# Kernel optimization log

Measured on AMD Instinct MI355X. Metric: run time of the kernel, lower is better.

Reference implementation:

```python
import jax, jax.numpy as jnp
import numpy as np

N = 100000
E = 640000
C = 128
ALPHA = 0.1
BETA = 0.5
RESIDUAL = False


def setup_inputs() -> dict:
    key = jax.random.key(0)
    k1, k2, k3, k4, k5 = jax.random.split(key, 5)
    stdv = 1.0 / np.sqrt(C)
    x = jax.random.normal(k1, (N, C), dtype=jnp.float32)
    init_x = jax.random.normal(k2, (N, C), dtype=jnp.float32)
    weight = jax.random.uniform(k3, (C, C), dtype=jnp.float32, minval=-stdv, maxval=stdv)
    edge_index = jax.random.randint(k4, (2, E), 0, N, dtype=jnp.int64)
    edge_attr = jax.random.uniform(k5, (E,), dtype=jnp.float32)
    return {"x": x, "edge_index": edge_index, "edge_attr": edge_attr,
            "init_x": init_x, "weight": weight}


def reference(x, edge_index, edge_attr, init_x, weight):
    row, col = edge_index[0], edge_index[1]
    # spmm: out[row] += edge_attr * x[col]  (gather-scale-scatter)
    msgs = edge_attr[:, None] * x[col]                 # [E, C]
    hidden = jax.ops.segment_sum(msgs, row, num_segments=x.shape[0])  # [N, C]
    hidden = (1.0 - ALPHA) * hidden + ALPHA * init_x
    h = BETA * jnp.matmul(hidden, weight) + (1.0 - BETA) * hidden
    if RESIDUAL:
        h = h + x
    return h
```

## Files before the change

kernel.cpp:

```cpp
#include <hip/hip_runtime.h>


#define ALPHA 0.1f
#define BETA  0.5f
#define C_DIM 128
#define PAD   32
#define WSCALE (32767.0f / 0.9f)
#define WDEC   (0.9f / 32767.0f)

typedef __attribute__((ext_vector_type(8))) short short8v;
typedef __attribute__((ext_vector_type(4))) float f32x4;

__device__ inline unsigned bf16rn(float f) {
    unsigned u = __float_as_uint(f);
    return (u + 0x7FFFu + ((u >> 16) & 1u)) >> 16;
}
__device__ inline unsigned pack2(float lo, float hi) {
    return bf16rn(lo) | (bf16rn(hi) << 16);
}

__global__ void k_prep(const float4* __restrict__ x4, uint4* __restrict__ xb, int n8x,
                       const float* __restrict__ W, ushort* __restrict__ Wt,
                       const int* __restrict__ ei, const float* __restrict__ attr,
                       int* __restrict__ cnt, unsigned* __restrict__ recs, int E,
                       int nbin) {
    int b = blockIdx.x;
    if (b < nbin) {
        int base = b * 1024 + threadIdx.x;
#pragma unroll
        for (int k = 0; k < 4; ++k) {
            int e = base + k * 256;
            if (e < E) {
                int row = ei[e];
                int col = ei[E + e];
                float w = (1.0f - ALPHA) * attr[e];
                int wb = (int)(w * WSCALE + 0.5f);
                if (wb > 32767) wb = 32767;
                if (wb < 0) wb = 0;
                int pos = atomicAdd(&cnt[row], 1);
                if (pos >= PAD) pos = PAD - 1;
                __builtin_nontemporal_store(((unsigned)col << 15) | (unsigned)wb,
                                            &recs[(size_t)row * PAD + pos]);
            }
        }
    } else {
        int i = (b - nbin) * 256 + threadIdx.x;
        if (i < n8x) {
            float4 a = x4[2 * i], c = x4[2 * i + 1];
            uint4 o;
            o.x = pack2(a.x, a.y); o.y = pack2(a.z, a.w);
            o.z = pack2(c.x, c.y); o.w = pack2(c.z, c.w);
            xb[i] = o;
        } else if (i < n8x + C_DIM * C_DIM) {
            int j = i - n8x;
            int n = j >> 7, k = j & 127;
            float v = BETA * W[k * C_DIM + n] + ((k == n) ? (1.0f - BETA) : 0.0f);
            Wt[j] = (ushort)bf16rn(v);
        }
    }
}

__device__ inline void fma8(float* acc, float a, uint4 v) {
    acc[0] += a * __uint_as_float(v.x << 16);
    acc[1] += a * __uint_as_float(v.x & 0xffff0000u);
    acc[2] += a * __uint_as_float(v.y << 16);
    acc[3] += a * __uint_as_float(v.y & 0xffff0000u);
    acc[4] += a * __uint_as_float(v.z << 16);
    acc[5] += a * __uint_as_float(v.z & 0xffff0000u);
    acc[6] += a * __uint_as_float(v.w << 16);
    acc[7] += a * __uint_as_float(v.w & 0xffff0000u);
}

template <int MODE>
__global__ __launch_bounds__(256)
void k_gather(const void* __restrict__ xsrc, const int* __restrict__ cnt,
              const unsigned* __restrict__ recs, uint4* __restrict__ hb, int N) {
    const int tid = threadIdx.x;
    long r = (long)blockIdx.x * 16 + (tid >> 4);
    if (r >= N) return;
    const int l = tid & 15;

    float acc[8] = {0.f, 0.f, 0.f, 0.f, 0.f, 0.f, 0.f, 0.f};
    int end = cnt[r];
    if (end > PAD) end = PAD;
    const uint4* rp = (const uint4*)(recs + (size_t)r * PAD);

    for (int k = 0; k < end; k += 8) {
        uint4 qa = rp[(k >> 2) + 0];
        uint4 qb = rp[(k >> 2) + 1];
        int   c0 = (int)(qa.x >> 15), c1 = (int)(qa.y >> 15);
        int   c2 = (int)(qa.z >> 15), c3 = (int)(qa.w >> 15);
        int   c4 = (int)(qb.x >> 15), c5 = (int)(qb.y >> 15);
        int   c6 = (int)(qb.z >> 15), c7 = (int)(qb.w >> 15);
        float w0 = (float)(qa.x & 0x7fffu) * WDEC;
        float w1 = (float)(qa.y & 0x7fffu) * WDEC;
        float w2 = (float)(qa.z & 0x7fffu) * WDEC;
        float w3 = (float)(qa.w & 0x7fffu) * WDEC;
        float w4 = (float)(qb.x & 0x7fffu) * WDEC;
        float w5 = (float)(qb.y & 0x7fffu) * WDEC;
        float w6 = (float)(qb.z & 0x7fffu) * WDEC;
        float w7 = (float)(qb.w & 0x7fffu) * WDEC;
        if (k + 1 >= end) { c1 = 0; w1 = 0.f; }
        if (k + 2 >= end) { c2 = 0; w2 = 0.f; }
        if (k + 3 >= end) { c3 = 0; w3 = 0.f; }
        if (k + 4 >= end) { c4 = 0; w4 = 0.f; }
        if (k + 5 >= end) { c5 = 0; w5 = 0.f; }
        if (k + 6 >= end) { c6 = 0; w6 = 0.f; }
        if (k + 7 >= end) { c7 = 0; w7 = 0.f; }
        if (MODE == 1) {
            const uint4* xb4 = (const uint4*)xsrc;
            uint4 v0 = xb4[(size_t)c0 * 16 + l];
            uint4 v1 = xb4[(size_t)c1 * 16 + l];
            uint4 v2 = xb4[(size_t)c2 * 16 + l];
            uint4 v3 = xb4[(size_t)c3 * 16 + l];
            uint4 v4 = xb4[(size_t)c4 * 16 + l];
            uint4 v5 = xb4[(size_t)c5 * 16 + l];
            uint4 v6 = xb4[(size_t)c6 * 16 + l];
            uint4 v7 = xb4[(size_t)c7 * 16 + l];
            fma8(acc, w0, v0); fma8(acc, w1, v1);
            fma8(acc, w2, v2); fma8(acc, w3, v3);
            fma8(acc, w4, v4); fma8(acc, w5, v5);
            fma8(acc, w6, v6); fma8(acc, w7, v7);
        } else {
            const float4* x4 = (const float4*)xsrc;
            int cc[8] = {c0, c1, c2, c3, c4, c5, c6, c7};
            float ww[8] = {w0, w1, w2, w3, w4, w5, w6, w7};
#pragma unroll
            for (int j = 0; j < 8; ++j) {
                const float4* xr = x4 + (size_t)cc[j] * 32 + 2 * l;
                float4 a0 = xr[0], a1 = xr[1];
                float w = ww[j];
                acc[0] += w * a0.x; acc[1] += w * a0.y;
                acc[2] += w * a0.z; acc[3] += w * a0.w;
                acc[4] += w * a1.x; acc[5] += w * a1.y;
                acc[6] += w * a1.z; acc[7] += w * a1.w;
            }
        }
    }
    uint4 o;
    o.x = pack2(acc[0], acc[1]);
    o.y = pack2(acc[2], acc[3]);
    o.z = pack2(acc[4], acc[5]);
    o.w = pack2(acc[6], acc[7]);
    hb[(size_t)r * 16 + l] = o;
}

__global__ __launch_bounds__(256)
void k_gemm(const uint4* __restrict__ hb, const float4* __restrict__ if4,
            const ushort* __restrict__ Wt, float* __restrict__ out, int N) {
    const uint4* W16 = (const uint4*)Wt;
    int lane = threadIdx.x & 63;
    int wv   = threadIdx.x >> 6;
    int m = lane & 15, g = lane >> 4;
    long R0 = (long)blockIdx.x * 128 + wv * 32;

    f32x4 acc[2][8];
#pragma unroll
    for (int t = 0; t < 2; ++t)
#pragma unroll
        for (int nt = 0; nt < 8; ++nt) acc[t][nt] = (f32x4){0.f, 0.f, 0.f, 0.f};

#pragma unroll
    for (int ks = 0; ks < 4; ++ks) {
        short8v a[2];
#pragma unroll
        for (int t = 0; t < 2; ++t) {
            long r = R0 + t * 16 + m;
            if (r >= N) r = N - 1;
            uint4 hv = hb[r * 16 + ks * 4 + g];
            float4 i0 = if4[r * 32 + ks * 8 + g * 2];
            float4 i1 = if4[r * 32 + ks * 8 + g * 2 + 1];
            float f0 = __uint_as_float(hv.x << 16)         + ALPHA * i0.x;
            float f1 = __uint_as_float(hv.x & 0xffff0000u) + ALPHA * i0.y;
            float f2 = __uint_as_float(hv.y << 16)         + ALPHA * i0.z;
            float f3 = __uint_as_float(hv.y & 0xffff0000u) + ALPHA * i0.w;
            float f4 = __uint_as_float(hv.z << 16)         + ALPHA * i1.x;
            float f5 = __uint_as_float(hv.z & 0xffff0000u) + ALPHA * i1.y;
            float f6 = __uint_as_float(hv.w << 16)         + ALPHA * i1.z;
            float f7 = __uint_as_float(hv.w & 0xffff0000u) + ALPHA * i1.w;
            union { uint4 q; short8v v; } av;
            av.q.x = pack2(f0, f1); av.q.y = pack2(f2, f3);
            av.q.z = pack2(f4, f5); av.q.w = pack2(f6, f7);
            a[t] = av.v;
        }
#pragma unroll
        for (int nt = 0; nt < 8; ++nt) {
            union { uint4 q; short8v v; } b;
            b.q = W16[(nt * 16 + m) * 16 + (ks * 4 + g)];
            acc[0][nt] = __builtin_amdgcn_mfma_f32_16x16x32_bf16(a[0], b.v, acc[0][nt], 0, 0, 0);
            acc[1][nt] = __builtin_amdgcn_mfma_f32_16x16x32_bf16(a[1], b.v, acc[1][nt], 0, 0, 0);
        }
    }

#pragma unroll
    for (int t = 0; t < 2; ++t) {
        long rb = R0 + t * 16 + g * 4;
#pragma unroll
        for (int reg = 0; reg < 4; ++reg) {
            long r = rb + reg;
            if (r >= N) continue;
            float* outp = out + r * C_DIM + m;
#pragma unroll
            for (int nt = 0; nt < 8; ++nt) outp[nt * 16] = acc[t][nt][reg];
        }
    }
}

extern "C" void kernel_launch(void* const* d_in, const int* in_sizes, int n_in,
                              void* d_out, int out_size, void* d_ws, size_t ws_size,
                              hipStream_t stream) {
    const float* x      = (const float*)d_in[0];
    const int*   ei     = (const int*)d_in[1];
    const float* attr   = (const float*)d_in[2];
    const float* init_x = (const float*)d_in[3];
    const float* W      = (const float*)d_in[4];
    float* out = (float*)d_out;

    const int N = in_sizes[0] / C_DIM;
    const int E = in_sizes[2];

    const int N_pad = (N + 255) & ~255;
    const size_t cnt_bytes = (size_t)N_pad * 4;
    const size_t rec_bytes = (size_t)N * PAD * 4;
    const size_t wt_bytes  = (size_t)C_DIM * C_DIM * 2;
    const size_t xb_bytes  = (size_t)N * C_DIM * 2;
    const size_t hb_bytes  = (size_t)N * C_DIM * 2;
    const size_t base_need = cnt_bytes + rec_bytes + wt_bytes + hb_bytes;

    const int mode = (ws_size >= base_need + xb_bytes) ? 1 : 0;

    char* wsp = (char*)d_ws;
    int*      cnt  = (int*)wsp;
    unsigned* recs = (unsigned*)(wsp + cnt_bytes);
    ushort*   Wt   = (ushort*)((char*)recs + rec_bytes);
    uint4*    hb   = (uint4*)((char*)Wt + wt_bytes);
    uint4*    xb   = (mode == 1) ? (uint4*)((char*)hb + hb_bytes) : nullptr;

    const int n8x = (mode == 1) ? (N * C_DIM / 8) : 0;
    const int nbin  = (E + 1023) / 1024;
    const int nconv = (n8x + C_DIM * C_DIM + 255) / 256;

    hipMemsetAsync(cnt, 0, (size_t)N * 4, stream);
    k_prep<<<nbin + nconv, 256, 0, stream>>>(
        (const float4*)x, xb, n8x, W, Wt, ei, attr, cnt, recs, E, nbin);

    if (mode == 1) {
        k_gather<1><<<(N + 15) / 16, 256, 0, stream>>>((const void*)xb, cnt, recs, hb, N);
    } else {
        k_gather<0><<<(N + 15) / 16, 256, 0, stream>>>((const void*)x, cnt, recs, hb, N);
    }
    k_gemm<<<(N + 127) / 128, 256, 0, stream>>>(hb, (const float4*)init_x, Wt, out, N);
}
```

Measured before the change: 119.7 us.

## Replace global-atomic ELL binning with two-pass bucketed partition and LDS ELL build

Edge binning into per-row ELL slots is split into two kernels. The first counting-sorts each 4096-edge chunk into 512-row buckets using shared-memory atomics and writes bucketed records plus offsets. The second builds each bucket's ELL block in LDS and writes it out coalesced, which removes global atomics, scattered nontemporal stores and the count memset. This adds an extra kernel launch and a slab round-trip through global memory that reuses the hidden-buffer space. nbuck can reach 196, so it still fits the 256-entry shared arrays.

```diff
diff --git a/kernel.cpp b/kernel.cpp
--- a/kernel.cpp
+++ b/kernel.cpp
@@ -5,6 +5,8 @@
 #define BETA  0.5f
 #define C_DIM 128
 #define PAD   32
+#define EB    4096
+#define RB    512
 #define WSCALE (32767.0f / 0.9f)
 #define WDEC   (0.9f / 32767.0f)
 
@@ -19,32 +21,56 @@
     return bf16rn(lo) | (bf16rn(hi) << 16);
 }
 
-__global__ void k_prep(const float4* __restrict__ x4, uint4* __restrict__ xb, int n8x,
-                       const float* __restrict__ W, ushort* __restrict__ Wt,
-                       const int* __restrict__ ei, const float* __restrict__ attr,
-                       int* __restrict__ cnt, unsigned* __restrict__ recs, int E,
-                       int nbin) {
+__global__ __launch_bounds__(256)
+void k_part(const int* __restrict__ ei, const float* __restrict__ attr,
+            const float4* __restrict__ x4, uint4* __restrict__ xb, int n8x,
+            const float* __restrict__ W, ushort* __restrict__ Wt,
+            uint2* __restrict__ slab, int* __restrict__ off,
+            int E, int nbin, int nbuck) {
     int b = blockIdx.x;
+    int t = threadIdx.x;
     if (b < nbin) {
-        int base = b * 1024 + threadIdx.x;
-#pragma unroll
-        for (int k = 0; k < 4; ++k) {
-            int e = base + k * 256;
-            if (e < E) {
-                int row = ei[e];
-                int col = ei[E + e];
-                float w = (1.0f - ALPHA) * attr[e];
-                int wb = (int)(w * WSCALE + 0.5f);
-                if (wb > 32767) wb = 32767;
-                if (wb < 0) wb = 0;
-                int pos = atomicAdd(&cnt[row], 1);
-                if (pos >= PAD) pos = PAD - 1;
-                __builtin_nontemporal_store(((unsigned)col << 15) | (unsigned)wb,
-                                            &recs[(size_t)row * PAD + pos]);
-            }
+        __shared__ int cnt_s[256];
+        __shared__ int pre_s[256];
+        cnt_s[t] = 0;
+        __syncthreads();
+        int e0 = b * EB;
+        int eend = (e0 + EB < E) ? e0 + EB : E;
+        for (int e = e0 + t; e < eend; e += 256)
+            atomicAdd(&cnt_s[ei[e] >> 9], 1);
+        __syncthreads();
+        int v = cnt_s[t];
+        pre_s[t] = v;
+        for (int d = 1; d < 256; d <<= 1) {
+            __syncthreads();
+            int tmp = (t >= d) ? pre_s[t - d] : 0;
+            __syncthreads();
+            pre_s[t] += tmp;
+        }
+        __syncthreads();
+        int excl = pre_s[t] - v;
+        __syncthreads();
+        pre_s[t] = excl;
+        cnt_s[t] = 0;
+        if (t < nbuck) off[b * (nbuck + 1) + t] = e0 + excl;
+        if (t == 0)    off[b * (nbuck + 1) + nbuck] = eend;
+        __syncthreads();
+        for (int e = e0 + t; e < eend; e += 256) {
+            int row = ei[e];
+            int col = ei[E + e];
+            float w = (1.0f - ALPHA) * attr[e];
+            int wb = (int)(w * WSCALE + 0.5f);
+            if (wb > 32767) wb = 32767;
+            if (wb < 0) wb = 0;
+            int bk = row >> 9;
+            int rank = atomicAdd(&cnt_s[bk], 1);
+            uint2 rec;
+            rec.x = ((unsigned)col << 15) | (unsigned)wb;
+            rec.y = (unsigned)row;
+            slab[e0 + pre_s[bk] + rank] = rec;
         }
     } else {
-        int i = (b - nbin) * 256 + threadIdx.x;
+        int i = (b - nbin) * 256 + t;
         if (i < n8x) {
             float4 a = x4[2 * i], c = x4[2 * i + 1];
             uint4 o;
@@ -57,6 +83,40 @@
             float v = BETA * W[k * C_DIM + n] + ((k == n) ? (1.0f - BETA) : 0.0f);
             Wt[j] = (ushort)bf16rn(v);
         }
+    }
+}
+
+__global__ __launch_bounds__(256)
+void k_ell(const uint2* __restrict__ slab, const int* __restrict__ off,
+           int nbin, int nbuck, unsigned* __restrict__ recs,
+           int* __restrict__ cnt, int N) {
+    __shared__ int deg[RB];
+    __shared__ unsigned ell[RB * PAD];
+    int t = threadIdx.x;
+    int beta = blockIdx.x;
+    int r0 = beta * RB;
+    for (int i = t; i < RB; i += 256) deg[i] = 0;
+    __syncthreads();
+    int wv = t >> 6, ln = t & 63;
+    for (int s = wv; s < nbin; s += 4) {
+        int st = off[s * (nbuck + 1) + beta];
+        int en = off[s * (nbuck + 1) + beta + 1];
+        for (int i = st + ln; i < en; i += 64) {
+            uint2 rc = slab[i];
+            int rl = (int)rc.y - r0;
+            int rank = atomicAdd(&deg[rl], 1);
+            if (rank < PAD) ell[rl * PAD + rank] = rc.x;
+        }
+    }
+    __syncthreads();
+    int nrows = N - r0;
+    if (nrows > RB) nrows = RB;
+    if (nrows <= 0) return;
+    for (int i = t; i < nrows * PAD; i += 256)
+        recs[(size_t)r0 * PAD + i] = ell[i];
+    for (int i = t; i < nrows; i += 256) {
+        int d = deg[i];
+        cnt[r0 + i] = (d > PAD) ? PAD : d;
     }
 }
 
@@ -219,13 +279,20 @@
     const int N = in_sizes[0] / C_DIM;
     const int E = in_sizes[2];
 
+    const int nbin  = (E + EB - 1) / EB;
+    const int nbuck = (N + RB - 1) / RB;
+
     const int N_pad = (N + 255) & ~255;
-    const size_t cnt_bytes = (size_t)N_pad * 4;
-    const size_t rec_bytes = (size_t)N * PAD * 4;
-    const size_t wt_bytes  = (size_t)C_DIM * C_DIM * 2;
-    const size_t xb_bytes  = (size_t)N * C_DIM * 2;
-    const size_t hb_bytes  = (size_t)N * C_DIM * 2;
-    const size_t base_need = cnt_bytes + rec_bytes + wt_bytes + hb_bytes;
+    const size_t cnt_bytes  = (size_t)N_pad * 4;
+    const size_t rec_bytes  = (size_t)nbuck * RB * PAD * 4;
+    const size_t wt_bytes   = (size_t)C_DIM * C_DIM * 2;
+    const size_t hb_bytes   = (size_t)N * C_DIM * 2;
+    const size_t xb_bytes   = (size_t)N * C_DIM * 2;
+    const size_t slab_bytes = (size_t)(nbin * EB) * 8;
+    const size_t off_bytes  = (size_t)nbin * (nbuck + 1) * 4;
+    const size_t base_need  = cnt_bytes + rec_bytes + wt_bytes +
+                              ((hb_bytes > slab_bytes + off_bytes) ? hb_bytes
+                                                                   : slab_bytes + off_bytes);
 
     const int mode = (ws_size >= base_need + xb_bytes) ? 1 : 0;
 
@@ -233,16 +300,20 @@
     int*      cnt  = (int*)wsp;
     unsigned* recs = (unsigned*)(wsp + cnt_bytes);
     ushort*   Wt   = (ushort*)((char*)recs + rec_bytes);
-    uint4*    hb   = (uint4*)((char*)Wt + wt_bytes);
-    uint4*    xb   = (mode == 1) ? (uint4*)((char*)hb + hb_bytes) : nullptr;
+    char*     hbr  = (char*)Wt + wt_bytes;
+    uint4*    hb   = (uint4*)hbr;
+    uint2*    slab = (uint2*)hbr;
+    int*      off  = (int*)(hbr + slab_bytes);
+    uint4*    xb   = (mode == 1) ? (uint4*)(hbr + ((hb_bytes > slab_bytes + off_bytes)
+                                                   ? hb_bytes : slab_bytes + off_bytes))
+                                 : nullptr;
 
     const int n8x = (mode == 1) ? (N * C_DIM / 8) : 0;
-    const int nbin  = (E + 1023) / 1024;
     const int nconv = (n8x + C_DIM * C_DIM + 255) / 256;
 
-    hipMemsetAsync(cnt, 0, (size_t)N * 4, stream);
-    k_prep<<<nbin + nconv, 256, 0, stream>>>(
-        (const float4*)x, xb, n8x, W, Wt, ei, attr, cnt, recs, E, nbin);
+    k_part<<<nbin + nconv, 256, 0, stream>>>(ei, attr, (const float4*)x, xb, n8x,
+                                             W, Wt, slab, off, E, nbin, nbuck);
+    k_ell<<<nbuck, 256, 0, stream>>>(slab, off, nbin, nbuck, recs, cnt, N);
 
     if (mode == 1) {
         k_gather<1><<<(N + 15) / 16, 256, 0, stream>>>((const void*)xb, cnt, recs, hb, N);
```

Result: faster. 116.6 us (-2.7%).
